# Kernel optimization log

Hardware: AMD Instinct MI355X
Metric: run time of the kernel (lower is better)

The kernel has to match this reference:

```python
import jax, jax.numpy as jnp
import numpy as np

N = 65536
IN_FEAT = 512
OUT_FEAT = 512
K = 16


def setup_inputs() -> dict:
    key = jax.random.key(0)
    k_feat, k_wt, k_wp, k_idx = jax.random.split(key, 4)
    feat = jax.random.normal(k_feat, (N, IN_FEAT), dtype=jnp.float32)
    # nn.Linear(in, out, bias=False): y = x @ W.T with W [out, in].
    # We store W as [in, out] so y = x @ W (same math, transposed layout).
    scale = 1.0 / np.sqrt(IN_FEAT)
    W_theta = jax.random.uniform(k_wt, (IN_FEAT, OUT_FEAT), dtype=jnp.float32, minval=-scale, maxval=scale)
    W_phi = jax.random.uniform(k_wp, (IN_FEAT, OUT_FEAT), dtype=jnp.float32, minval=-scale, maxval=scale)
    src_ind = jax.random.randint(k_idx, (N, K), 0, N, dtype=jnp.int64)
    return {"k": K, "src_ind": src_ind, "feat": feat, "W_theta": W_theta, "W_phi": W_phi}


def reference(k, src_ind, feat, W_theta, W_phi):
    # Dense projections (cuBLAS-friendly part)
    h_theta = feat @ W_theta            # [N, out]
    h_phi = feat @ W_phi                # [N, out]
    h_src = h_theta                     # message contribution from source node
    h_dst = h_phi - h_theta             # per-destination additive term
    # fused_edgeconv_op: result[i] = max_{j in 0..k} (h_src[src_ind[i, j]] + h_dst[i]).
    # h_dst[i] is constant over neighbors, so max commutes with the add:
    neigh = h_src[src_ind[:, :k]]       # [N, k, out] irregular gather
    result = jnp.max(neigh, axis=1) + h_dst  # [N, out]
    return result
```

## Files before the change

### kernel.cpp

```cpp
#include <hip/hip_runtime.h>
#include <hip/hip_bf16.h>
#include <stdint.h>


typedef __bf16 bf16x8 __attribute__((ext_vector_type(8)));
typedef float f32x4 __attribute__((ext_vector_type(4)));

__device__ __forceinline__ unsigned short f2bf(float x) {
    unsigned u = __float_as_uint(x);
    unsigned r = u + 0x7fffu + ((u >> 16) & 1u);
    return (unsigned short)(r >> 16);
}

__device__ __forceinline__ void async_ld16(const void* g, void* l) {
    __builtin_amdgcn_global_load_lds(
        (const __attribute__((address_space(1))) unsigned int*)g,
        (__attribute__((address_space(3))) unsigned int*)l,
        16, 0, 0);
}

__global__ void k_convert_feat(const float* __restrict__ feat,
                               unsigned short* __restrict__ featb) {
    int i = (blockIdx.x * 256 + threadIdx.x) * 4;
    f32x4 f = __builtin_nontemporal_load((const f32x4*)(feat + i));
    ushort4 o;
    o.x = f2bf(f.x); o.y = f2bf(f.y); o.z = f2bf(f.z); o.w = f2bf(f.w);
    *(ushort4*)(featb + i) = o;
}

__global__ void k_prep_w(const float* __restrict__ Wth,
                         const float* __restrict__ Wph,
                         unsigned short* __restrict__ wtc) {
    __shared__ float tile[32][33];
    const int k0 = (blockIdx.x & 15) * 32;
    const int n0 = (blockIdx.x >> 4) * 32;
    const int t  = threadIdx.x;
    const int cc = t & 31;
    const int r0 = t >> 5;
#pragma unroll
    for (int it = 0; it < 4; ++it) {
        const int r  = it * 8 + r0;
        const int gn = n0 + cc;
        float v;
        if (gn < 512) v = Wth[(k0 + r) * 512 + gn];
        else          v = Wph[(k0 + r) * 512 + (gn - 512)] - Wth[(k0 + r) * 512 + (gn - 512)];
        tile[r][cc] = v;
    }
    __syncthreads();
#pragma unroll
    for (int it = 0; it < 4; ++it) {
        const int r2 = t & 31;
        const int c2 = it * 8 + (t >> 5);
        wtc[(size_t)(n0 + c2) * 512 + k0 + r2] = f2bf(tile[r2][c2]);
    }
}

__global__ __launch_bounds__(256, 3)
void k_gemm(const unsigned short* __restrict__ A,
            const unsigned short* __restrict__ Bt,
            unsigned short* __restrict__ theta,
            float* __restrict__ delta_f,
            size_t slabStride)
{
    __shared__ __align__(16) unsigned short As[2][128 * 32];
    __shared__ __align__(16) unsigned short Bs[2][128 * 32];

    const int tid  = threadIdx.x;
    const int wave = tid >> 6;
    const int lane = tid & 63;
    const int quad = lane >> 4;
    const int l15  = lane & 15;

    const int b  = blockIdx.x;
    const int mt = (b >> 6) * 8 + (b & 7);
    const int nt = (b >> 3) & 7;
    const int m0 = mt * 128;
    const int n0 = nt * 128;

    const int wm = wave >> 1;
    const int wn = wave & 1;

    f32x4 acc[4][4];
#pragma unroll
    for (int i = 0; i < 4; i++)
#pragma unroll
        for (int j = 0; j < 4; j++) acc[i][j] = (f32x4){0.f, 0.f, 0.f, 0.f};

    const int r0   = (wave * 2 + 0) * 16 + (lane >> 2);
    const int r1   = (wave * 2 + 1) * 16 + (lane >> 2);
    const int koff = (lane & 3) * 8;

    const unsigned short* Ag0 = A  + (size_t)(m0 + r0) * 512 + koff;
    const unsigned short* Ag1 = A  + (size_t)(m0 + r1) * 512 + koff;
    const unsigned short* Bg0 = Bt + (size_t)(n0 + r0) * 512 + koff;
    const unsigned short* Bg1 = Bt + (size_t)(n0 + r1) * 512 + koff;

    unsigned short* const sA = &As[0][0];
    unsigned short* const sB = &Bs[0][0];
    const int oA0 = (wave * 2 + 0) * 512;
    const int oA1 = (wave * 2 + 1) * 512;

#define STAGE(buf, kg) do {                              \
        async_ld16(Ag0 + (kg), sA + (buf) * 4096 + oA0); \
        async_ld16(Ag1 + (kg), sA + (buf) * 4096 + oA1); \
        async_ld16(Bg0 + (kg), sB + (buf) * 4096 + oA0); \
        async_ld16(Bg1 + (kg), sB + (buf) * 4096 + oA1); \
    } while (0)

    STAGE(0, 0);
    __syncthreads();

#pragma unroll
    for (int kt = 0; kt < 16; ++kt) {
        const int cur = kt & 1;
        if (kt < 15) STAGE(cur ^ 1, (kt + 1) * 32);

        bf16x8 af[4], bfr[4];
#pragma unroll
        for (int t = 0; t < 4; ++t) {
            const int am = wm * 64 + t * 16 + l15;
            af[t]  = *(const bf16x8*)&sA[cur * 4096 + am * 32 + quad * 8];
            const int bn = wn * 64 + t * 16 + l15;
            bfr[t] = *(const bf16x8*)&sB[cur * 4096 + bn * 32 + quad * 8];
        }
#pragma unroll
        for (int i = 0; i < 4; i++)
#pragma unroll
            for (int j = 0; j < 4; j++)
                acc[i][j] = __builtin_amdgcn_mfma_f32_16x16x32_bf16(bfr[j], af[i], acc[i][j], 0, 0, 0);

        if (kt < 15) __syncthreads();
    }
#undef STAGE

    const bool is_theta = (n0 < 512);
#pragma unroll
    for (int i = 0; i < 4; i++) {
        const int m = m0 + wm * 64 + i * 16 + l15;
#pragma unroll
        for (int j = 0; j < 4; j++) {
            const int nb = n0 + wn * 64 + j * 16 + quad * 4;
            const f32x4 v = acc[i][j];
            if (is_theta) {
                ushort4 o;
                o.x = f2bf(v[0]); o.y = f2bf(v[1]);
                o.z = f2bf(v[2]); o.w = f2bf(v[3]);
                *(ushort4*)&theta[(size_t)(nb >> 5) * slabStride
                                  + (size_t)m * 32 + (nb & 31)] = o;
            } else {
                *(f32x4*)&delta_f[(size_t)m * 512 + (nb - 512)] = v;
            }
        }
    }
}

__global__ void k_gather(const unsigned short* __restrict__ theta,
                         float* out,
                         const int* __restrict__ src,
                         const int* __restrict__ kptr,
                         size_t slabStride)
{
    const int b     = blockIdx.x;
    const int xcd   = b & 7;
    const int chunk = b >> 3;
    const int kk    = *kptr;

    const int tid = threadIdx.x;
    const int c8  = (tid & 3) * 8;
    const int rly = tid >> 2;

    for (int half = 0; half < 2; ++half) {
        const int slice = half * 8 + xcd;
        const unsigned short* slab = theta + (size_t)slice * slabStride;

#pragma unroll 2
        for (int pass = 0; pass < 4; ++pass) {
            const int row = chunk * 256 + pass * 64 + rly;

            float m0 = -INFINITY, m1 = -INFINITY, m2 = -INFINITY, m3 = -INFINITY;
            float m4 = -INFINITY, m5 = -INFINITY, m6 = -INFINITY, m7 = -INFINITY;

            if (kk == 16) {
                const int4* sp = (const int4*)(src + (size_t)row * 16);
                int4 sv[4];
                sv[0] = sp[0]; sv[1] = sp[1]; sv[2] = sp[2]; sv[3] = sp[3];
#pragma unroll
                for (int q = 0; q < 4; ++q) {
                    const int ss[4] = {sv[q].x, sv[q].y, sv[q].z, sv[q].w};
#pragma unroll
                    for (int j = 0; j < 4; ++j) {
                        const uint4 v = *(const uint4*)(slab + (size_t)ss[j] * 32 + c8);
                        m0 = fmaxf(m0, __uint_as_float(v.x << 16));
                        m1 = fmaxf(m1, __uint_as_float(v.x & 0xffff0000u));
                        m2 = fmaxf(m2, __uint_as_float(v.y << 16));
                        m3 = fmaxf(m3, __uint_as_float(v.y & 0xffff0000u));
                        m4 = fmaxf(m4, __uint_as_float(v.z << 16));
                        m5 = fmaxf(m5, __uint_as_float(v.z & 0xffff0000u));
                        m6 = fmaxf(m6, __uint_as_float(v.w << 16));
                        m7 = fmaxf(m7, __uint_as_float(v.w & 0xffff0000u));
                    }
                }
            } else {
                for (int k = 0; k < kk; ++k) {
                    const int s = src[(size_t)row * 16 + k];
                    const uint4 v = *(const uint4*)(slab + (size_t)s * 32 + c8);
                    m0 = fmaxf(m0, __uint_as_float(v.x << 16));
                    m1 = fmaxf(m1, __uint_as_float(v.x & 0xffff0000u));
                    m2 = fmaxf(m2, __uint_as_float(v.y << 16));
                    m3 = fmaxf(m3, __uint_as_float(v.y & 0xffff0000u));
                    m4 = fmaxf(m4, __uint_as_float(v.z << 16));
                    m5 = fmaxf(m5, __uint_as_float(v.z & 0xffff0000u));
                    m6 = fmaxf(m6, __uint_as_float(v.w << 16));
                    m7 = fmaxf(m7, __uint_as_float(v.w & 0xffff0000u));
                }
            }

            float* op = out + (size_t)row * 512 + slice * 32 + c8;
            const f32x4 d0 = __builtin_nontemporal_load((const f32x4*)op);
            const f32x4 d1 = __builtin_nontemporal_load((const f32x4*)op + 1);
            f32x4 o0, o1;
            o0[0] = m0 + d0[0]; o0[1] = m1 + d0[1]; o0[2] = m2 + d0[2]; o0[3] = m3 + d0[3];
            o1[0] = m4 + d1[0]; o1[1] = m5 + d1[1]; o1[2] = m6 + d1[2]; o1[3] = m7 + d1[3];
            __builtin_nontemporal_store(o0, (f32x4*)op);
            __builtin_nontemporal_store(o1, (f32x4*)op + 1);
        }
    }
}

extern "C" void kernel_launch(void* const* d_in, const int* in_sizes, int n_in,
                              void* d_out, int out_size, void* d_ws, size_t ws_size,
                              hipStream_t stream) {
    const int*   kptr = (const int*)d_in[0];
    const int*   src  = (const int*)d_in[1];
    const float* feat = (const float*)d_in[2];
    const float* Wth  = (const float*)d_in[3];
    const float* Wph  = (const float*)d_in[4];
    float* out = (float*)d_out;

    const int N = in_sizes[2] / 512;
    const size_t slabStride = (size_t)N * 32;

    unsigned short* featb = (unsigned short*)d_ws;
    unsigned short* wtc   = (unsigned short*)((char*)d_ws + (size_t)64 * 1024 * 1024);
    unsigned short* table = (unsigned short*)((char*)d_ws + (size_t)65 * 1024 * 1024);

    k_convert_feat<<<(N * 512) / 1024, 256, 0, stream>>>(feat, featb);
    k_prep_w<<<512, 256, 0, stream>>>(Wth, Wph, wtc);
    k_gemm<<<(N / 128) * 8, 256, 0, stream>>>(featb, wtc, table, out, slabStride);
    k_gather<<<8 * (N / 256), 256, 0, stream>>>(table, out, src, kptr, slabStride);
}
```

Measured before the change: 489.9 us.

## Triple-buffer GEMM LDS staging and reschedule gather so each block owns one slice

The GEMM moves from double to triple-buffered async global-to-LDS loads. Explicit vmcnt waits and raw s_barrier replace __syncthreads, so two k-tiles stay in flight and the wait before each barrier is shorter. The gather kernel now gives each block a single 32-column slice over 512 rows, where before one block handled two slices over 256 rows, with the slice chosen by launch phase so all blocks touching a slab run together for L2 locality. The cost is more LDS per block (48KB, which may limit occupancy at 3 blocks per CU) and hand-written waitcnt logic that must match the number of outstanding loads.

New measurement: 458.8 us. -6.4%, faster.

```diff
diff --git a/kernel.cpp b/kernel.cpp
--- a/kernel.cpp
+++ b/kernel.cpp
@@ -62,8 +62,8 @@
             float* __restrict__ delta_f,
             size_t slabStride)
 {
-    __shared__ __align__(16) unsigned short As[2][128 * 32];
-    __shared__ __align__(16) unsigned short Bs[2][128 * 32];
+    __shared__ __align__(16) unsigned short As[3][128 * 32];
+    __shared__ __align__(16) unsigned short Bs[3][128 * 32];
 
     const int tid  = threadIdx.x;
     const int wave = tid >> 6;
@@ -95,33 +95,33 @@
     const unsigned short* Bg0 = Bt + (size_t)(n0 + r0) * 512 + koff;
     const unsigned short* Bg1 = Bt + (size_t)(n0 + r1) * 512 + koff;
 
-    unsigned short* const sA = &As[0][0];
-    unsigned short* const sB = &Bs[0][0];
     const int oA0 = (wave * 2 + 0) * 512;
     const int oA1 = (wave * 2 + 1) * 512;
 
-#define STAGE(buf, kg) do {                              \
-        async_ld16(Ag0 + (kg), sA + (buf) * 4096 + oA0); \
-        async_ld16(Ag1 + (kg), sA + (buf) * 4096 + oA1); \
-        async_ld16(Bg0 + (kg), sB + (buf) * 4096 + oA0); \
-        async_ld16(Bg1 + (kg), sB + (buf) * 4096 + oA1); \
+#define STAGE(buf, kg) do {                            \
+        async_ld16(Ag0 + (kg), &As[(buf)][oA0]);       \
+        async_ld16(Ag1 + (kg), &As[(buf)][oA1]);       \
+        async_ld16(Bg0 + (kg), &Bs[(buf)][oA0]);       \
+        async_ld16(Bg1 + (kg), &Bs[(buf)][oA1]);       \
     } while (0)
 
     STAGE(0, 0);
-    __syncthreads();
+    STAGE(1, 32);
+    asm volatile("s_waitcnt vmcnt(4)" ::: "memory");
+    __builtin_amdgcn_s_barrier();
 
 #pragma unroll
     for (int kt = 0; kt < 16; ++kt) {
-        const int cur = kt & 1;
-        if (kt < 15) STAGE(cur ^ 1, (kt + 1) * 32);
+        const int cur = kt % 3;
+        if (kt < 14) STAGE((kt + 2) % 3, (kt + 2) * 32);
 
         bf16x8 af[4], bfr[4];
 #pragma unroll
         for (int t = 0; t < 4; ++t) {
             const int am = wm * 64 + t * 16 + l15;
-            af[t]  = *(const bf16x8*)&sA[cur * 4096 + am * 32 + quad * 8];
+            af[t]  = *(const bf16x8*)&As[cur][am * 32 + quad * 8];
             const int bn = wn * 64 + t * 16 + l15;
-            bfr[t] = *(const bf16x8*)&sB[cur * 4096 + bn * 32 + quad * 8];
+            bfr[t] = *(const bf16x8*)&Bs[cur][bn * 32 + quad * 8];
         }
 #pragma unroll
         for (int i = 0; i < 4; i++)
@@ -129,7 +129,12 @@
             for (int j = 0; j < 4; j++)
                 acc[i][j] = __builtin_amdgcn_mfma_f32_16x16x32_bf16(bfr[j], af[i], acc[i][j], 0, 0, 0);
 
-        if (kt < 15) __syncthreads();
+        if (kt < 15) {
+            __builtin_amdgcn_sched_barrier(0);
+            if (kt < 14) asm volatile("s_waitcnt vmcnt(4)" ::: "memory");
+            else         asm volatile("s_waitcnt vmcnt(0)" ::: "memory");
+            __builtin_amdgcn_s_barrier();
+        }
     }
 #undef STAGE
 
@@ -158,52 +163,38 @@
                          float* out,
                          const int* __restrict__ src,
                          const int* __restrict__ kptr,
-                         size_t slabStride)
+                         int chunksPerSlice, size_t slabStride)
 {
     const int b     = blockIdx.x;
     const int xcd   = b & 7;
-    const int chunk = b >> 3;
+    const int t2    = b >> 3;
+    const int chunk = t2 % chunksPerSlice;
+    const int phase = t2 / chunksPerSlice;
+    const int slice = phase * 8 + xcd;
     const int kk    = *kptr;
 
+    const unsigned short* slab = theta + (size_t)slice * slabStride;
     const int tid = threadIdx.x;
     const int c8  = (tid & 3) * 8;
     const int rly = tid >> 2;
 
-    for (int half = 0; half < 2; ++half) {
-        const int slice = half * 8 + xcd;
-        const unsigned short* slab = theta + (size_t)slice * slabStride;
-
 #pragma unroll 2
-        for (int pass = 0; pass < 4; ++pass) {
-            const int row = chunk * 256 + pass * 64 + rly;
-
-            float m0 = -INFINITY, m1 = -INFINITY, m2 = -INFINITY, m3 = -INFINITY;
-            float m4 = -INFINITY, m5 = -INFINITY, m6 = -INFINITY, m7 = -INFINITY;
-
-            if (kk == 16) {
-                const int4* sp = (const int4*)(src + (size_t)row * 16);
-                int4 sv[4];
-                sv[0] = sp[0]; sv[1] = sp[1]; sv[2] = sp[2]; sv[3] = sp[3];
-#pragma unroll
-                for (int q = 0; q < 4; ++q) {
-                    const int ss[4] = {sv[q].x, sv[q].y, sv[q].z, sv[q].w};
-#pragma unroll
-                    for (int j = 0; j < 4; ++j) {
-                        const uint4 v = *(const uint4*)(slab + (size_t)ss[j] * 32 + c8);
-                        m0 = fmaxf(m0, __uint_as_float(v.x << 16));
-                        m1 = fmaxf(m1, __uint_as_float(v.x & 0xffff0000u));
-                        m2 = fmaxf(m2, __uint_as_float(v.y << 16));
-                        m3 = fmaxf(m3, __uint_as_float(v.y & 0xffff0000u));
-                        m4 = fmaxf(m4, __uint_as_float(v.z << 16));
-                        m5 = fmaxf(m5, __uint_as_float(v.z & 0xffff0000u));
-                        m6 = fmaxf(m6, __uint_as_float(v.w << 16));
-                        m7 = fmaxf(m7, __uint_as_float(v.w & 0xffff0000u));
-                    }
-                }
-            } else {
-                for (int k = 0; k < kk; ++k) {
-                    const int s = src[(size_t)row * 16 + k];
-                    const uint4 v = *(const uint4*)(slab + (size_t)s * 32 + c8);
+    for (int pass = 0; pass < 8; ++pass) {
+        const int row = chunk * 512 + pass * 64 + rly;
+
+        float m0 = -INFINITY, m1 = -INFINITY, m2 = -INFINITY, m3 = -INFINITY;
+        float m4 = -INFINITY, m5 = -INFINITY, m6 = -INFINITY, m7 = -INFINITY;
+
+        if (kk == 16) {
+            const int4* sp = (const int4*)(src + (size_t)row * 16);
+            int4 sv[4];
+            sv[0] = sp[0]; sv[1] = sp[1]; sv[2] = sp[2]; sv[3] = sp[3];
+#pragma unroll
+            for (int q = 0; q < 4; ++q) {
+                const int ss[4] = {sv[q].x, sv[q].y, sv[q].z, sv[q].w};
+#pragma unroll
+                for (int j = 0; j < 4; ++j) {
+                    const uint4 v = *(const uint4*)(slab + (size_t)ss[j] * 32 + c8);
                     m0 = fmaxf(m0, __uint_as_float(v.x << 16));
                     m1 = fmaxf(m1, __uint_as_float(v.x & 0xffff0000u));
                     m2 = fmaxf(m2, __uint_as_float(v.y << 16));
@@ -214,16 +205,29 @@
                     m7 = fmaxf(m7, __uint_as_float(v.w & 0xffff0000u));
                 }
             }
-
-            float* op = out + (size_t)row * 512 + slice * 32 + c8;
-            const f32x4 d0 = __builtin_nontemporal_load((const f32x4*)op);
-            const f32x4 d1 = __builtin_nontemporal_load((const f32x4*)op + 1);
-            f32x4 o0, o1;
-            o0[0] = m0 + d0[0]; o0[1] = m1 + d0[1]; o0[2] = m2 + d0[2]; o0[3] = m3 + d0[3];
-            o1[0] = m4 + d1[0]; o1[1] = m5 + d1[1]; o1[2] = m6 + d1[2]; o1[3] = m7 + d1[3];
-            __builtin_nontemporal_store(o0, (f32x4*)op);
-            __builtin_nontemporal_store(o1, (f32x4*)op + 1);
-        }
+        } else {
+            for (int k = 0; k < kk; ++k) {
+                const int s = src[(size_t)row * 16 + k];
+                const uint4 v = *(const uint4*)(slab + (size_t)s * 32 + c8);
+                m0 = fmaxf(m0, __uint_as_float(v.x << 16));
+                m1 = fmaxf(m1, __uint_as_float(v.x & 0xffff0000u));
+                m2 = fmaxf(m2, __uint_as_float(v.y << 16));
+                m3 = fmaxf(m3, __uint_as_float(v.y & 0xffff0000u));
+                m4 = fmaxf(m4, __uint_as_float(v.z << 16));
+                m5 = fmaxf(m5, __uint_as_float(v.z & 0xffff0000u));
+                m6 = fmaxf(m6, __uint_as_float(v.w << 16));
+                m7 = fmaxf(m7, __uint_as_float(v.w & 0xffff0000u));
+            }
+        }
+
+        float* op = out + (size_t)row * 512 + slice * 32 + c8;
+        const f32x4 d0 = __builtin_nontemporal_load((const f32x4*)op);
+        const f32x4 d1 = __builtin_nontemporal_load((const f32x4*)op + 1);
+        f32x4 o0, o1;
+        o0[0] = m0 + d0[0]; o0[1] = m1 + d0[1]; o0[2] = m2 + d0[2]; o0[3] = m3 + d0[3];
+        o1[0] = m4 + d1[0]; o1[1] = m5 + d1[1]; o1[2] = m6 + d1[2]; o1[3] = m7 + d1[3];
+        __builtin_nontemporal_store(o0, (f32x4*)op);
+        __builtin_nontemporal_store(o1, (f32x4*)op + 1);
     }
 }
 
@@ -244,8 +248,11 @@
     unsigned short* wtc   = (unsigned short*)((char*)d_ws + (size_t)64 * 1024 * 1024);
     unsigned short* table = (unsigned short*)((char*)d_ws + (size_t)65 * 1024 * 1024);
 
+    const int chunksPerSlice = N / 512;
+
     k_convert_feat<<<(N * 512) / 1024, 256, 0, stream>>>(feat, featb);
     k_prep_w<<<512, 256, 0, stream>>>(Wth, Wph, wtc);
     k_gemm<<<(N / 128) * 8, 256, 0, stream>>>(featb, wtc, table, out, slabStride);
-    k_gather<<<8 * (N / 256), 256, 0, stream>>>(table, out, src, kptr, slabStride);
-}
+    k_gather<<<16 * chunksPerSlice, 256, 0, stream>>>(table, out, src, kptr,
+                                                      chunksPerSlice, slabStride);
+}
```

## Fuse fp32-to-bf16 feature conversion into GEMM A-tile loading and split gather launches

Applied to the files above, without the earlier changes.

Removes the separate feature conversion kernel. The GEMM now reads fp32 feature rows directly into registers, converts them to bf16 and writes them into a swizzled LDS layout, while B tiles still use async LDS DMA with matching XOR swizzled offsets. This avoids writing and re-reading a 64 MB bf16 copy of the features, at the cost of twice the global read volume for A inside the GEMM and extra conversion work in its loop. The gather is also split into two launches, one per half of the column slices, in place of a loop inside one kernel.

After: 493.1 us. About the same (+0.7%).

```diff
diff --git a/kernel.cpp b/kernel.cpp
--- a/kernel.cpp
+++ b/kernel.cpp
@@ -5,6 +5,7 @@
 
 typedef __bf16 bf16x8 __attribute__((ext_vector_type(8)));
 typedef float f32x4 __attribute__((ext_vector_type(4)));
+typedef unsigned short u16x8 __attribute__((ext_vector_type(8)));
 
 __device__ __forceinline__ unsigned short f2bf(float x) {
     unsigned u = __float_as_uint(x);
@@ -17,15 +18,6 @@
         (const __attribute__((address_space(1))) unsigned int*)g,
         (__attribute__((address_space(3))) unsigned int*)l,
         16, 0, 0);
-}
-
-__global__ void k_convert_feat(const float* __restrict__ feat,
-                               unsigned short* __restrict__ featb) {
-    int i = (blockIdx.x * 256 + threadIdx.x) * 4;
-    f32x4 f = __builtin_nontemporal_load((const f32x4*)(feat + i));
-    ushort4 o;
-    o.x = f2bf(f.x); o.y = f2bf(f.y); o.z = f2bf(f.z); o.w = f2bf(f.w);
-    *(ushort4*)(featb + i) = o;
 }
 
 __global__ void k_prep_w(const float* __restrict__ Wth,
@@ -56,7 +48,7 @@
 }
 
 __global__ __launch_bounds__(256, 3)
-void k_gemm(const unsigned short* __restrict__ A,
+void k_gemm(const float* __restrict__ A,
             const unsigned short* __restrict__ Bt,
             unsigned short* __restrict__ theta,
             float* __restrict__ delta_f,
@@ -86,42 +78,68 @@
 #pragma unroll
         for (int j = 0; j < 4; j++) acc[i][j] = (f32x4){0.f, 0.f, 0.f, 0.f};
 
-    const int r0   = (wave * 2 + 0) * 16 + (lane >> 2);
-    const int r1   = (wave * 2 + 1) * 16 + (lane >> 2);
-    const int koff = (lane & 3) * 8;
-
-    const unsigned short* Ag0 = A  + (size_t)(m0 + r0) * 512 + koff;
-    const unsigned short* Ag1 = A  + (size_t)(m0 + r1) * 512 + koff;
-    const unsigned short* Bg0 = Bt + (size_t)(n0 + r0) * 512 + koff;
-    const unsigned short* Bg1 = Bt + (size_t)(n0 + r1) * 512 + koff;
-
-    unsigned short* const sA = &As[0][0];
-    unsigned short* const sB = &Bs[0][0];
-    const int oA0 = (wave * 2 + 0) * 512;
-    const int oA1 = (wave * 2 + 1) * 512;
-
-#define STAGE(buf, kg) do {                              \
-        async_ld16(Ag0 + (kg), sA + (buf) * 4096 + oA0); \
-        async_ld16(Ag1 + (kg), sA + (buf) * 4096 + oA1); \
-        async_ld16(Bg0 + (kg), sB + (buf) * 4096 + oA0); \
-        async_ld16(Bg1 + (kg), sB + (buf) * 4096 + oA1); \
+    const int r0 = wave * 32 + (lane >> 2);
+    const int r1 = r0 + 16;
+    const int sw = (((lane & 3) ^ ((lane >> 3) & 3)) << 3);
+
+    const float* Ag0 = A + (size_t)(m0 + r0) * 512 + (lane & 3) * 8;
+    const float* Ag1 = A + (size_t)(m0 + r1) * 512 + (lane & 3) * 8;
+    const unsigned short* Bg0 = Bt + (size_t)(n0 + r0) * 512 + sw;
+    const unsigned short* Bg1 = Bt + (size_t)(n0 + r1) * 512 + sw;
+
+    const int wAo0 = r0 * 32 + sw;
+    const int wAo1 = r1 * 32 + sw;
+    const int oB0  = wave * 1024;
+    const int oB1  = wave * 1024 + 512;
+
+    f32x4 a0lo, a0hi, a1lo, a1hi;
+
+#define DMAB(buf, kg) do {                              \
+        async_ld16(Bg0 + (kg), &Bs[(buf)][oB0]);        \
+        async_ld16(Bg1 + (kg), &Bs[(buf)][oB1]);        \
     } while (0)
-
-    STAGE(0, 0);
+#define ALOAD(kg) do {                                  \
+        a0lo = *(const f32x4*)(Ag0 + (kg));             \
+        a0hi = *(const f32x4*)(Ag0 + (kg) + 4);         \
+        a1lo = *(const f32x4*)(Ag1 + (kg));             \
+        a1hi = *(const f32x4*)(Ag1 + (kg) + 4);         \
+    } while (0)
+#define ACVTW(buf) do {                                                       \
+        u16x8 p0, p1;                                                         \
+        p0[0] = f2bf(a0lo[0]); p0[1] = f2bf(a0lo[1]);                         \
+        p0[2] = f2bf(a0lo[2]); p0[3] = f2bf(a0lo[3]);                         \
+        p0[4] = f2bf(a0hi[0]); p0[5] = f2bf(a0hi[1]);                         \
+        p0[6] = f2bf(a0hi[2]); p0[7] = f2bf(a0hi[3]);                         \
+        p1[0] = f2bf(a1lo[0]); p1[1] = f2bf(a1lo[1]);                         \
+        p1[2] = f2bf(a1lo[2]); p1[3] = f2bf(a1lo[3]);                         \
+        p1[4] = f2bf(a1hi[0]); p1[5] = f2bf(a1hi[1]);                         \
+        p1[6] = f2bf(a1hi[2]); p1[7] = f2bf(a1hi[3]);                         \
+        *(u16x8*)&As[(buf)][wAo0] = p0;                                       \
+        *(u16x8*)&As[(buf)][wAo1] = p1;                                       \
+    } while (0)
+
+    DMAB(0, 0);
+    ALOAD(0);
+    ACVTW(0);
     __syncthreads();
+
+    const int rdoff = (quad << 3) ^ (((l15 >> 1) & 3) << 3);
 
 #pragma unroll
     for (int kt = 0; kt < 16; ++kt) {
         const int cur = kt & 1;
-        if (kt < 15) STAGE(cur ^ 1, (kt + 1) * 32);
+        if (kt < 15) {
+            DMAB(cur ^ 1, (kt + 1) * 32);
+            ALOAD((kt + 1) * 32);
+        }
 
         bf16x8 af[4], bfr[4];
 #pragma unroll
         for (int t = 0; t < 4; ++t) {
             const int am = wm * 64 + t * 16 + l15;
-            af[t]  = *(const bf16x8*)&sA[cur * 4096 + am * 32 + quad * 8];
+            af[t]  = *(const bf16x8*)&As[cur][am * 32 + rdoff];
             const int bn = wn * 64 + t * 16 + l15;
-            bfr[t] = *(const bf16x8*)&sB[cur * 4096 + bn * 32 + quad * 8];
+            bfr[t] = *(const bf16x8*)&Bs[cur][bn * 32 + rdoff];
         }
 #pragma unroll
         for (int i = 0; i < 4; i++)
@@ -129,9 +147,14 @@
             for (int j = 0; j < 4; j++)
                 acc[i][j] = __builtin_amdgcn_mfma_f32_16x16x32_bf16(bfr[j], af[i], acc[i][j], 0, 0, 0);
 
-        if (kt < 15) __syncthreads();
-    }
-#undef STAGE
+        if (kt < 15) {
+            ACVTW(cur ^ 1);
+            __syncthreads();
+        }
+    }
+#undef DMAB
+#undef ALOAD
+#undef ACVTW
 
     const bool is_theta = (n0 < 512);
 #pragma unroll
@@ -158,52 +181,36 @@
                          float* out,
                          const int* __restrict__ src,
                          const int* __restrict__ kptr,
-                         size_t slabStride)
+                         int phase, size_t slabStride)
 {
     const int b     = blockIdx.x;
     const int xcd   = b & 7;
     const int chunk = b >> 3;
+    const int slice = phase * 8 + xcd;
     const int kk    = *kptr;
 
+    const unsigned short* slab = theta + (size_t)slice * slabStride;
     const int tid = threadIdx.x;
     const int c8  = (tid & 3) * 8;
     const int rly = tid >> 2;
 
-    for (int half = 0; half < 2; ++half) {
-        const int slice = half * 8 + xcd;
-        const unsigned short* slab = theta + (size_t)slice * slabStride;
-
 #pragma unroll 2
-        for (int pass = 0; pass < 4; ++pass) {
-            const int row = chunk * 256 + pass * 64 + rly;
-
-            float m0 = -INFINITY, m1 = -INFINITY, m2 = -INFINITY, m3 = -INFINITY;
-            float m4 = -INFINITY, m5 = -INFINITY, m6 = -INFINITY, m7 = -INFINITY;
-
-            if (kk == 16) {
-                const int4* sp = (const int4*)(src + (size_t)row * 16);
-                int4 sv[4];
-                sv[0] = sp[0]; sv[1] = sp[1]; sv[2] = sp[2]; sv[3] = sp[3];
-#pragma unroll
-                for (int q = 0; q < 4; ++q) {
-                    const int ss[4] = {sv[q].x, sv[q].y, sv[q].z, sv[q].w};
-#pragma unroll
-                    for (int j = 0; j < 4; ++j) {
-                        const uint4 v = *(const uint4*)(slab + (size_t)ss[j] * 32 + c8);
-                        m0 = fmaxf(m0, __uint_as_float(v.x << 16));
-                        m1 = fmaxf(m1, __uint_as_float(v.x & 0xffff0000u));
-                        m2 = fmaxf(m2, __uint_as_float(v.y << 16));
-                        m3 = fmaxf(m3, __uint_as_float(v.y & 0xffff0000u));
-                        m4 = fmaxf(m4, __uint_as_float(v.z << 16));
-                        m5 = fmaxf(m5, __uint_as_float(v.z & 0xffff0000u));
-                        m6 = fmaxf(m6, __uint_as_float(v.w << 16));
-                        m7 = fmaxf(m7, __uint_as_float(v.w & 0xffff0000u));
-                    }
-                }
-            } else {
-                for (int k = 0; k < kk; ++k) {
-                    const int s = src[(size_t)row * 16 + k];
-                    const uint4 v = *(const uint4*)(slab + (size_t)s * 32 + c8);
+    for (int pass = 0; pass < 4; ++pass) {
+        const int row = chunk * 256 + pass * 64 + rly;
+
+        float m0 = -INFINITY, m1 = -INFINITY, m2 = -INFINITY, m3 = -INFINITY;
+        float m4 = -INFINITY, m5 = -INFINITY, m6 = -INFINITY, m7 = -INFINITY;
+
+        if (kk == 16) {
+            const int4* sp = (const int4*)(src + (size_t)row * 16);
+            int4 sv[4];
+            sv[0] = sp[0]; sv[1] = sp[1]; sv[2] = sp[2]; sv[3] = sp[3];
+#pragma unroll
+            for (int q = 0; q < 4; ++q) {
+                const int ss[4] = {sv[q].x, sv[q].y, sv[q].z, sv[q].w};
+#pragma unroll
+                for (int j = 0; j < 4; ++j) {
+                    const uint4 v = *(const uint4*)(slab + (size_t)ss[j] * 32 + c8);
                     m0 = fmaxf(m0, __uint_as_float(v.x << 16));
                     m1 = fmaxf(m1, __uint_as_float(v.x & 0xffff0000u));
                     m2 = fmaxf(m2, __uint_as_float(v.y << 16));
@@ -214,16 +221,29 @@
                     m7 = fmaxf(m7, __uint_as_float(v.w & 0xffff0000u));
                 }
             }
-
-            float* op = out + (size_t)row * 512 + slice * 32 + c8;
-            const f32x4 d0 = __builtin_nontemporal_load((const f32x4*)op);
-            const f32x4 d1 = __builtin_nontemporal_load((const f32x4*)op + 1);
-            f32x4 o0, o1;
-            o0[0] = m0 + d0[0]; o0[1] = m1 + d0[1]; o0[2] = m2 + d0[2]; o0[3] = m3 + d0[3];
-            o1[0] = m4 + d1[0]; o1[1] = m5 + d1[1]; o1[2] = m6 + d1[2]; o1[3] = m7 + d1[3];
-            __builtin_nontemporal_store(o0, (f32x4*)op);
-            __builtin_nontemporal_store(o1, (f32x4*)op + 1);
-        }
+        } else {
+            for (int k = 0; k < kk; ++k) {
+                const int s = src[(size_t)row * 16 + k];
+                const uint4 v = *(const uint4*)(slab + (size_t)s * 32 + c8);
+                m0 = fmaxf(m0, __uint_as_float(v.x << 16));
+                m1 = fmaxf(m1, __uint_as_float(v.x & 0xffff0000u));
+                m2 = fmaxf(m2, __uint_as_float(v.y << 16));
+                m3 = fmaxf(m3, __uint_as_float(v.y & 0xffff0000u));
+                m4 = fmaxf(m4, __uint_as_float(v.z << 16));
+                m5 = fmaxf(m5, __uint_as_float(v.z & 0xffff0000u));
+                m6 = fmaxf(m6, __uint_as_float(v.w << 16));
+                m7 = fmaxf(m7, __uint_as_float(v.w & 0xffff0000u));
+            }
+        }
+
+        float* op = out + (size_t)row * 512 + slice * 32 + c8;
+        const f32x4 d0 = __builtin_nontemporal_load((const f32x4*)op);
+        const f32x4 d1 = __builtin_nontemporal_load((const f32x4*)op + 1);
+        f32x4 o0, o1;
+        o0[0] = m0 + d0[0]; o0[1] = m1 + d0[1]; o0[2] = m2 + d0[2]; o0[3] = m3 + d0[3];
+        o1[0] = m4 + d1[0]; o1[1] = m5 + d1[1]; o1[2] = m6 + d1[2]; o1[3] = m7 + d1[3];
+        __builtin_nontemporal_store(o0, (f32x4*)op);
+        __builtin_nontemporal_store(o1, (f32x4*)op + 1);
     }
 }
 
@@ -240,12 +260,11 @@
     const int N = in_sizes[2] / 512;
     const size_t slabStride = (size_t)N * 32;
 
-    unsigned short* featb = (unsigned short*)d_ws;
-    unsigned short* wtc   = (unsigned short*)((char*)d_ws + (size_t)64 * 1024 * 1024);
-    unsigned short* table = (unsigned short*)((char*)d_ws + (size_t)65 * 1024 * 1024);
-
-    k_convert_feat<<<(N * 512) / 1024, 256, 0, stream>>>(feat, featb);
+    unsigned short* wtc   = (unsigned short*)d_ws;
+    unsigned short* table = (unsigned short*)((char*)d_ws + (size_t)16 * 1024 * 1024);
+
     k_prep_w<<<512, 256, 0, stream>>>(Wth, Wph, wtc);
-    k_gemm<<<(N / 128) * 8, 256, 0, stream>>>(featb, wtc, table, out, slabStride);
-    k_gather<<<8 * (N / 256), 256, 0, stream>>>(table, out, src, kptr, slabStride);
-}
+    k_gemm<<<(N / 128) * 8, 256, 0, stream>>>(feat, wtc, table, out, slabStride);
+    k_gather<<<8 * (N / 256), 256, 0, stream>>>(table, out, src, kptr, 0, slabStride);
+    k_gather<<<8 * (N / 256), 256, 0, stream>>>(table, out, src, kptr, 1, slabStride);
+}
```
